# Kernel tuning notes

Hardware: AMD Instinct MI355X
Metric: run time of the kernel (lower is better)

The kernel has to match this reference:

```python
import jax, jax.numpy as jnp
import numpy as np
import math

BS = 8
ROI = 512
D = 1024     # box_feat_dim
G = 16       # group
DH = D // G  # group_feat_dim = 64
GEO = 64     # geo_feat_dim


def setup_inputs() -> dict:
    key = jax.random.key(0)
    ks = jax.random.split(key, 12)
    n = BS * ROI
    box_appearance_feat = jax.random.normal(ks[0], (n, D), dtype=jnp.float32)
    # valid boxes: x2 > x1, y2 > y1, w > 0 (needed for log(w / w^T))
    x1 = jax.random.uniform(ks[1], (n, 1), minval=0.0, maxval=0.5)
    y1 = jax.random.uniform(ks[2], (n, 1), minval=0.0, maxval=0.5)
    w = jax.random.uniform(ks[3], (n, 1), minval=0.05, maxval=0.5)
    h = jax.random.uniform(ks[4], (n, 1), minval=0.05, maxval=0.5)
    boxes = jnp.concatenate([x1, y1, x1 + w, y1 + h], axis=1)
    sc = lambda fan: 1.0 / math.sqrt(fan)
    W_geo = jax.random.normal(ks[5], (GEO, 4), dtype=jnp.float32) * sc(4)
    b_geo = jnp.zeros((GEO,), dtype=jnp.float32)
    W_bgc = jax.random.normal(ks[6], (G, GEO), dtype=jnp.float32) * sc(GEO)  # 1x1 conv GEO->G
    b_bgc = jnp.zeros((G,), dtype=jnp.float32)
    W_q = jax.random.normal(ks[7], (D, D), dtype=jnp.float32) * sc(D)
    b_q = jnp.zeros((D,), dtype=jnp.float32)
    W_k = jax.random.normal(ks[8], (D, D), dtype=jnp.float32) * sc(D)
    b_k = jnp.zeros((D,), dtype=jnp.float32)
    # grouped 1x1 conv G*D -> D with groups=G: per-group linear D -> DH
    W_gc = jax.random.normal(ks[9], (G, DH, D), dtype=jnp.float32) * sc(D)
    b_gc = jnp.zeros((D,), dtype=jnp.float32)
    return {
        "box_appearance_feat": box_appearance_feat, "boxes": boxes,
        "W_geo": W_geo, "b_geo": b_geo, "W_bgc": W_bgc, "b_bgc": b_bgc,
        "W_q": W_q, "b_q": b_q, "W_k": W_k, "b_k": b_k,
        "W_gc": W_gc, "b_gc": b_gc, "bs": BS,
    }


def geometric_encoding(boxes):
    # boxes: [bs, N, 4] -> [bs, N, N, 4]
    x1, y1, x2, y2 = (boxes[..., i] for i in range(4))  # [bs, N]
    w = x2 - x1
    h = y2 - y1
    cx = 0.5 * (x1 + x2)
    cy = 0.5 * (y1 + y2)
    # row-wise division by w_i (torch broadcasts [N,1] over columns)
    dx = (cx[:, :, None] - cx[:, None, :]) / w[:, :, None]
    dx = jnp.log(jnp.maximum(jnp.abs(dx), 1e-3))
    dy = (cy[:, :, None] - cy[:, None, :]) / w[:, :, None]
    dy = jnp.log(jnp.maximum(jnp.abs(dy), 1e-3))
    dw = jnp.log(w[:, :, None] / w[:, None, :])
    dh = jnp.log(h[:, :, None] / h[:, None, :])
    return jnp.stack([dx, dy, dw, dh], axis=-1)


def reference(box_appearance_feat, boxes, W_geo, b_geo, W_bgc, b_bgc,
              W_q, b_q, W_k, b_k, W_gc, b_gc, bs):
    n_total = box_appearance_feat.shape[0]
    roi = n_total // bs
    enc = geometric_encoding(boxes.reshape(bs, roi, 4))            # [b, i, j, 4]
    geo = jnp.tanh(enc @ W_geo.T + b_geo)                          # [b, i, j, GEO]
    # 1x1 conv (GEO -> G) + ReLU (mmcv ConvModule default act), then permute to [b, i, g, j]
    geo_wg = jax.nn.relu(jnp.einsum('bijd,gd->bigj', geo, W_bgc)
                         + b_bgc[None, None, :, None])
    x = box_appearance_feat.reshape(bs, roi, D)
    q = (x @ W_q.T + b_q).reshape(bs, roi, G, DH)
    k = (x @ W_k.T + b_k).reshape(bs, roi, G, DH)
    logits = jnp.einsum('bngd,bmgd->bngm', q, k) / math.sqrt(DH)   # [b, n, g, m]
    weighted = jnp.log(jnp.maximum(geo_wg, 1e-6)) + logits
    sm = jax.nn.softmax(weighted, axis=-1)                         # [b, n, g, m]
    out = jnp.einsum('bngm,bmd->bngd', sm, x)                      # [b, n, g, D]
    # grouped 1x1 conv (G*D -> D, groups=G) + ReLU
    out = jax.nn.relu(jnp.einsum('bngd,god->bngo', out, W_gc)
                      + b_gc.reshape(G, DH))
    return out.reshape(bs * roi, D)
```

## Files before the change

kernel.cpp:

```cpp
#include <hip/hip_runtime.h>
#include <math.h>
#include <stdint.h>


using f16   = _Float16;
using f16x4 = __attribute__((ext_vector_type(4))) f16;
using f16x8 = __attribute__((ext_vector_type(8))) f16;
using f32x4 = __attribute__((ext_vector_type(4))) float;

__device__ __forceinline__ float hw_exp2(float x) { return __builtin_amdgcn_exp2f(x); }
__device__ __forceinline__ float hw_log2(float x) { return __builtin_amdgcn_logf(x); }

__device__ __forceinline__ void cp16(void* lds, const void* g) {
    __builtin_amdgcn_global_load_lds(
        (const __attribute__((address_space(1))) uint32_t*)g,
        (__attribute__((address_space(3))) uint32_t*)lds, 16, 0, 0);
}

__global__ __launch_bounds__(256) void geom_kernel(
    const float* __restrict__ boxes,
    float* __restrict__ gcx, float* __restrict__ gcy,
    float* __restrict__ gw,  float* __restrict__ glw, float* __restrict__ glh)
{
    const int i = blockIdx.x * 256 + threadIdx.x;
    if (i >= 4096) return;
    const float x1 = boxes[i * 4 + 0];
    const float y1 = boxes[i * 4 + 1];
    const float x2 = boxes[i * 4 + 2];
    const float y2 = boxes[i * 4 + 3];
    const float w = x2 - x1, h = y2 - y1;
    gcx[i] = 0.5f * (x1 + x2);
    gcy[i] = 0.5f * (y1 + y2);
    gw[i]  = w;
    glw[i] = logf(w);
    glh[i] = logf(h);
}

__global__ __launch_bounds__(256) void ab_kernel(
    const float* __restrict__ glw, const float* __restrict__ glh,
    const float* __restrict__ W_geo, const float* __restrict__ b_geo,
    float* __restrict__ ABa, float* __restrict__ ABb)
{
    const int i = (blockIdx.x << 2) + (threadIdx.x >> 6);
    const int d = threadIdx.x & 63;
    const float4 wr = *reinterpret_cast<const float4*>(W_geo + (d << 2));
    const float lw = glw[i], lh = glh[i];
    const float bv = fmaf(lw, wr.z, lh * wr.w);
    ABb[i * 64 + d] = bv;
    ABa[i * 64 + d] = bv + b_geo[d] - lw * (wr.x + wr.y);
}

__device__ __forceinline__ void pack_row1(const float* __restrict__ src,
                                          f16* __restrict__ dst, int m, int tid)
{
    const int k = tid << 2;
    const float4 v = *reinterpret_cast<const float4*>(src + (size_t)m * 1024 + k);
    f16x4 a;
    a[0] = (f16)v.x; a[1] = (f16)v.y; a[2] = (f16)v.z; a[3] = (f16)v.w;
    const int sw = (m & 7) << 3;
    *reinterpret_cast<f16x4*>(dst + (size_t)m * 1024 + (k & ~63) + ((k & 63) ^ sw)) = a;
}

__global__ __launch_bounds__(256) void pack4_kernel(
    const float* __restrict__ x,  const float* __restrict__ Wq,
    const float* __restrict__ Wk, const float* __restrict__ Wg,
    f16* __restrict__ xs, f16* __restrict__ wqs,
    f16* __restrict__ wks, f16* __restrict__ wgs)
{
    const int bid = blockIdx.x;
    const float* src; f16* dst; int m;
    if (bid < 4096)      { src = x;  dst = xs;  m = bid; }
    else if (bid < 5120) { src = Wq; dst = wqs; m = bid - 4096; }
    else if (bid < 6144) { src = Wk; dst = wks; m = bid - 5120; }
    else                 { src = Wg; dst = wgs; m = bid - 6144; }
    pack_row1(src, dst, m, threadIdx.x);
}

__global__ __launch_bounds__(256) void packqk_kernel(
    const float* __restrict__ qws, const float* __restrict__ kws,
    f16* __restrict__ qp, f16* __restrict__ kp)
{
    const int bid = blockIdx.x;
    if (bid < 4096) pack_row1(qws, qp, bid, threadIdx.x);
    else            pack_row1(kws, kp, bid - 4096, threadIdx.x);
}

__global__ __launch_bounds__(256) void gemm_qk_f16(
    const f16* __restrict__ xs, const f16* __restrict__ wqs, const f16* __restrict__ wks,
    const float* __restrict__ b_q, const float* __restrict__ b_k,
    float* __restrict__ qout, float* __restrict__ kout)
{
    const bool isK = (blockIdx.z != 0);
    const f16* Bmat   = isK ? wks : wqs;
    const float* bias = isK ? b_k : b_q;
    float* C          = isK ? kout : qout;
    const int m0 = blockIdx.y << 7;
    const int n0 = blockIdx.x << 7;

    __shared__ f16 As[8192];
    __shared__ f16 Bs[8192];

    const int tid  = threadIdx.x;
    const int lane = tid & 63;
    const int w    = tid >> 6;
    const int wr   = (w >> 1) << 6;
    const int wc   = (w & 1) << 6;
    const int srow = lane >> 3;
    const int sseg = (lane & 7) << 4;
    const int l15  = lane & 15;
    const int kgrp = (lane >> 4) << 3;

    f32x4 acc[4][4] = {};

    int aoff[4], boff[4];
    #pragma unroll
    for (int f = 0; f < 4; ++f) {
        const int ra = wr + (f << 4) + l15;
        aoff[f] = (ra << 6) + (kgrp ^ ((ra & 7) << 3));
        const int rb = wc + (f << 4) + l15;
        boff[f] = (rb << 6) + (kgrp ^ ((rb & 7) << 3));
    }

    for (int s = 0; s < 16; ++s) {
        const size_t gb = (size_t)(s << 7) + sseg;
        #pragma unroll
        for (int it = 0; it < 4; ++it) {
            const int ch = (w << 2) + it;
            const int gr = (ch << 3) + srow;
            cp16((char*)As + (ch << 10), (const char*)xs   + (size_t)(m0 + gr) * 2048 + gb);
            cp16((char*)Bs + (ch << 10), (const char*)Bmat + (size_t)(n0 + gr) * 2048 + gb);
        }
        __syncthreads();

        f16x8 a0[4], a1[4], b0[4], b1[4];
        #pragma unroll
        for (int f = 0; f < 4; ++f) {
            a0[f] = *reinterpret_cast<const f16x8*>(As + aoff[f]);
            a1[f] = *reinterpret_cast<const f16x8*>(As + (aoff[f] ^ 32));
            b0[f] = *reinterpret_cast<const f16x8*>(Bs + boff[f]);
            b1[f] = *reinterpret_cast<const f16x8*>(Bs + (boff[f] ^ 32));
        }
        #pragma unroll
        for (int i = 0; i < 4; ++i)
            #pragma unroll
            for (int j = 0; j < 4; ++j) {
                acc[i][j] = __builtin_amdgcn_mfma_f32_16x16x32_f16(a0[i], b0[j], acc[i][j], 0, 0, 0);
                acc[i][j] = __builtin_amdgcn_mfma_f32_16x16x32_f16(a1[i], b1[j], acc[i][j], 0, 0, 0);
            }
        __syncthreads();
    }

    const int rgrp = (lane >> 4) << 2;
    #pragma unroll
    for (int j = 0; j < 4; ++j) {
        const int col = n0 + wc + (j << 4) + l15;
        const float bv = bias[col];
        #pragma unroll
        for (int i = 0; i < 4; ++i) {
            const int row = m0 + wr + (i << 4) + rgrp;
            #pragma unroll
            for (int r = 0; r < 4; ++r)
                C[(size_t)(row + r) * 1024 + col] = acc[i][j][r] + bv;
        }
    }
}

__global__ __launch_bounds__(256) void gemm_yt_f16(
    const f16* __restrict__ xs, const f16* __restrict__ wgs,
    f16* __restrict__ Yt)
{
    const int z = blockIdx.z;
    const int b = z >> 4, g = z & 15;
    const int m0 = blockIdx.y << 7;
    const f16* A    = xs  + (size_t)(b << 9) * 1024;
    const f16* Bmat = wgs + (size_t)(g << 6) * 1024;

    __shared__ f16 As[8192];
    __shared__ f16 Bs[4096];

    const int tid  = threadIdx.x;
    const int lane = tid & 63;
    const int w    = tid >> 6;
    const int wr   = (w >> 1) << 6;
    const int wc   = (w & 1) << 5;
    const int srow = lane >> 3;
    const int sseg = (lane & 7) << 4;
    const int l15  = lane & 15;
    const int kgrp = (lane >> 4) << 3;

    f32x4 acc[4][2] = {};

    int aoff[4], boff[2];
    #pragma unroll
    for (int f = 0; f < 4; ++f) {
        const int ra = wr + (f << 4) + l15;
        aoff[f] = (ra << 6) + (kgrp ^ ((ra & 7) << 3));
    }
    #pragma unroll
    for (int f = 0; f < 2; ++f) {
        const int rb = wc + (f << 4) + l15;
        boff[f] = (rb << 6) + (kgrp ^ ((rb & 7) << 3));
    }

    for (int s = 0; s < 16; ++s) {
        const size_t gb = (size_t)(s << 7) + sseg;
        #pragma unroll
        for (int it = 0; it < 4; ++it) {
            const int ch = (w << 2) + it;
            cp16((char*)As + (ch << 10),
                 (const char*)A + (size_t)(m0 + (ch << 3) + srow) * 2048 + gb);
        }
        #pragma unroll
        for (int it = 0; it < 2; ++it) {
            const int ch = (w << 1) + it;
            cp16((char*)Bs + (ch << 10),
                 (const char*)Bmat + (size_t)((ch << 3) + srow) * 2048 + gb);
        }
        __syncthreads();

        f16x8 a0[4], a1[4], b0[2], b1[2];
        #pragma unroll
        for (int f = 0; f < 4; ++f) {
            a0[f] = *reinterpret_cast<const f16x8*>(As + aoff[f]);
            a1[f] = *reinterpret_cast<const f16x8*>(As + (aoff[f] ^ 32));
        }
        #pragma unroll
        for (int f = 0; f < 2; ++f) {
            b0[f] = *reinterpret_cast<const f16x8*>(Bs + boff[f]);
            b1[f] = *reinterpret_cast<const f16x8*>(Bs + (boff[f] ^ 32));
        }
        #pragma unroll
        for (int i = 0; i < 4; ++i)
            #pragma unroll
            for (int j = 0; j < 2; ++j) {
                acc[i][j] = __builtin_amdgcn_mfma_f32_16x16x32_f16(b0[j], a0[i], acc[i][j], 0, 0, 0);
                acc[i][j] = __builtin_amdgcn_mfma_f32_16x16x32_f16(b1[j], a1[i], acc[i][j], 0, 0, 0);
            }
        __syncthreads();
    }

    const int rgrp = (lane >> 4) << 2;
    #pragma unroll
    for (int jj = 0; jj < 2; ++jj) {
        const int obase = wc + (jj << 4) + rgrp;
        #pragma unroll
        for (int i = 0; i < 4; ++i) {
            const int jcol = m0 + wr + (i << 4) + l15;
            const int jhi = (jcol >> 6) << 6, jlo = jcol & 63;
            #pragma unroll
            for (int r = 0; r < 4; ++r) {
                const int o = obase + r;
                Yt[((size_t)z << 15) + (o << 9) + jhi + (jlo ^ ((o & 7) << 3))]
                    = (f16)acc[i][jj][r];
            }
        }
    }
}

__global__ __launch_bounds__(256, 4) void geo_mfma(
    const float* __restrict__ gcx, const float* __restrict__ gcy,
    const float* __restrict__ gw,
    const float* __restrict__ ABa, const float* __restrict__ ABb,
    const float* __restrict__ W_geo, const float* __restrict__ W_bgc,
    const float* __restrict__ b_bgc,
    f16* __restrict__ S)
{
    __shared__ float2 sJ[512];

    const int tid  = threadIdx.x;
    const int lane = tid & 63;
    const int h    = lane >> 4;
    const int p    = lane & 15;
    const int w    = tid >> 6;
    const int bb   = blockIdx.y;
    const int irow = (blockIdx.x << 2) + w;
    const int ig   = (bb << 9) + irow;
    const float LN2 = 0.69314718056f;

    float2 wA[8], wB[8];
    #pragma unroll
    for (int e = 0; e < 8; ++e) {
        const float4 t0 = *reinterpret_cast<const float4*>(W_geo + (((h << 3) + e) << 2));
        wA[e] = make_float2(t0.x * LN2, t0.y * LN2);
        const float4 t1 = *reinterpret_cast<const float4*>(W_geo + ((32 + (h << 3) + e) << 2));
        wB[e] = make_float2(t1.x * LN2, t1.y * LN2);
    }
    float aiA[8], aiB[8];
    {
        const float4 a0 = *reinterpret_cast<const float4*>(ABa + ig * 64 + (h << 3));
        const float4 a1 = *reinterpret_cast<const float4*>(ABa + ig * 64 + (h << 3) + 4);
        aiA[0] = a0.x; aiA[1] = a0.y; aiA[2] = a0.z; aiA[3] = a0.w;
        aiA[4] = a1.x; aiA[5] = a1.y; aiA[6] = a1.z; aiA[7] = a1.w;
        const float4 b0 = *reinterpret_cast<const float4*>(ABa + ig * 64 + 32 + (h << 3));
        const float4 b1 = *reinterpret_cast<const float4*>(ABa + ig * 64 + 32 + (h << 3) + 4);
        aiB[0] = b0.x; aiB[1] = b0.y; aiB[2] = b0.z; aiB[3] = b0.w;
        aiB[4] = b1.x; aiB[5] = b1.y; aiB[6] = b1.z; aiB[7] = b1.w;
    }
    f16x8 wbh0, wbl0, wbh1, wbl1;
    #pragma unroll
    for (int e = 0; e < 8; ++e) {
        const float v0 = W_bgc[(p << 6) + (h << 3) + e];
        const f16 x0 = (f16)v0; wbh0[e] = x0; wbl0[e] = (f16)(v0 - (float)x0);
        const float v1 = W_bgc[(p << 6) + 32 + (h << 3) + e];
        const f16 x1 = (f16)v1; wbh1[e] = x1; wbl1[e] = (f16)(v1 - (float)x1);
    }
    const float bbias = b_bgc[p];
    const float cxi = gcx[ig], cyi = gcy[ig];
    const float ti  = 1e-3f * gw[ig];

    for (int l = tid; l < 512; l += 256) {
        const int jg = (bb << 9) + l;
        sJ[l] = make_float2(gcx[jg], gcy[jg]);
    }
    __syncthreads();

    const float* bjrow = ABb + ((size_t)(bb << 9) << 6) + (p << 6) + (h << 3);
    float4 cA0 = *reinterpret_cast<const float4*>(bjrow);
    float4 cA1 = *reinterpret_cast<const float4*>(bjrow + 4);
    float4 cB0 = *reinterpret_cast<const float4*>(bjrow + 32);
    float4 cB1 = *reinterpret_cast<const float4*>(bjrow + 36);

    f16* sp = S + (((size_t)((bb << 4) + p)) << 18) + ((size_t)irow << 9) + (h << 2);

    for (int jc = 0; jc < 32; ++jc) {
        float4 nA0, nA1, nB0, nB1;
        if (jc < 31) {
            const float* nx = bjrow + ((jc + 1) << 10);
            nA0 = *reinterpret_cast<const float4*>(nx);
            nA1 = *reinterpret_cast<const float4*>(nx + 4);
            nB0 = *reinterpret_cast<const float4*>(nx + 32);
            nB1 = *reinterpret_cast<const float4*>(nx + 36);
        }
        const float2 je = sJ[(jc << 4) + p];
        const float e0 = hw_log2(fmaxf(fabsf(cxi - je.x), ti));
        const float e1 = hw_log2(fmaxf(fabsf(cyi - je.y), ti));

        const float bjA[8] = {cA0.x, cA0.y, cA0.z, cA0.w, cA1.x, cA1.y, cA1.z, cA1.w};
        const float bjB[8] = {cB0.x, cB0.y, cB0.z, cB0.w, cB1.x, cB1.y, cB1.z, cB1.w};

        f16x8 hhA, hlA, hhB, hlB;
        #pragma unroll
        for (int e = 0; e < 8; ++e) {
            float t = fmaf(e0, wA[e].x, fmaf(e1, wA[e].y, aiA[e] - bjA[e]));
            t = fmaf(-2.0f, __builtin_amdgcn_rcpf(hw_exp2(t * 2.885390082f) + 1.0f), 1.0f);
            const f16 a = (f16)t; hhA[e] = a; hlA[e] = (f16)(t - (float)a);
            float u = fmaf(e0, wB[e].x, fmaf(e1, wB[e].y, aiB[e] - bjB[e]));
            u = fmaf(-2.0f, __builtin_amdgcn_rcpf(hw_exp2(u * 2.885390082f) + 1.0f), 1.0f);
            const f16 c = (f16)u; hhB[e] = c; hlB[e] = (f16)(u - (float)c);
        }
        f32x4 acc = {0.f, 0.f, 0.f, 0.f};
        acc = __builtin_amdgcn_mfma_f32_16x16x32_f16(hhA, wbh0, acc, 0, 0, 0);
        acc = __builtin_amdgcn_mfma_f32_16x16x32_f16(hlA, wbh0, acc, 0, 0, 0);
        acc = __builtin_amdgcn_mfma_f32_16x16x32_f16(hhA, wbl0, acc, 0, 0, 0);
        acc = __builtin_amdgcn_mfma_f32_16x16x32_f16(hhB, wbh1, acc, 0, 0, 0);
        acc = __builtin_amdgcn_mfma_f32_16x16x32_f16(hlB, wbh1, acc, 0, 0, 0);
        acc = __builtin_amdgcn_mfma_f32_16x16x32_f16(hhB, wbl1, acc, 0, 0, 0);

        f16x4 o4;
        #pragma unroll
        for (int r = 0; r < 4; ++r)
            o4[r] = (f16)fmaxf(acc[r] + bbias, 1e-6f);
        *reinterpret_cast<f16x4*>(sp + (jc << 4)) = o4;

        cA0 = nA0; cA1 = nA1; cB0 = nB0; cB1 = nB1;
    }
}

__global__ __launch_bounds__(256) void attn_fused(
    const f16* __restrict__ qp, const f16* __restrict__ kp,
    const f16* __restrict__ Sb, const f16* __restrict__ Yt,
    const float* __restrict__ b_gc, float* __restrict__ out)
{
    __shared__ float Ss[16][514];
    __shared__ f16   P[16 * 512];

    const int tid  = threadIdx.x;
    const int lane = tid & 63;
    const int w    = tid >> 6;
    const int h    = lane >> 4;
    const int p_   = lane & 15;
    const int kgrp = h << 3;
    const int i0   = blockIdx.x << 4;
    const int z    = blockIdx.y;
    const int b    = z >> 4, g = z & 15;

    const char* qbytes = (const char*)qp + ((size_t)((b << 9) + i0)) * 2048 + (g << 7);
    const char* kbytes = (const char*)kp + ((size_t)(b << 9)) * 2048 + (g << 7);

    f16x8 aq[2];
    {
        const char* qrow = qbytes + (size_t)p_ * 2048;
        #pragma unroll
        for (int s = 0; s < 2; ++s) {
            const int bo = ((s << 5) + kgrp) ^ ((p_ & 7) << 3);
            aq[s] = *reinterpret_cast<const f16x8*>(qrow + bo * 2);
        }
    }

    #pragma unroll
    for (int f = 0; f < 8; ++f) {
        const int j = (w << 7) + (f << 4) + p_;
        const char* krow = kbytes + (size_t)j * 2048;
        f32x4 a = {0.f, 0.f, 0.f, 0.f};
        #pragma unroll
        for (int s = 0; s < 2; ++s) {
            const int bo = ((s << 5) + kgrp) ^ ((j & 7) << 3);
            const f16x8 bk = *reinterpret_cast<const f16x8*>(krow + bo * 2);
            a = __builtin_amdgcn_mfma_f32_16x16x32_f16(aq[s], bk, a, 0, 0, 0);
        }
        #pragma unroll
        for (int r = 0; r < 4; ++r)
            Ss[(h << 2) + r][(w << 7) + (f << 4) + p_] = 0.125f * a[r];
    }
    __syncthreads();

    #pragma unroll
    for (int rr = 0; rr < 4; ++rr) {
        const int row = (w << 2) + rr;
        const f16* wbp = Sb + ((size_t)z << 18) + ((size_t)(i0 + row) << 9);
        float l[8];
        float m = -3.0e38f;
        #pragma unroll
        for (int t = 0; t < 8; ++t) { l[t] = Ss[row][(t << 6) + lane]; m = fmaxf(m, l[t]); }
        #pragma unroll
        for (int off = 32; off > 0; off >>= 1) m = fmaxf(m, __shfl_xor(m, off));
        float wb[8];
        #pragma unroll
        for (int t = 0; t < 8; ++t) wb[t] = (float)wbp[(t << 6) + lane];
        float ssum = 0.f;
        #pragma unroll
        for (int t = 0; t < 8; ++t) { l[t] = wb[t] * __expf(l[t] - m); ssum += l[t]; }
        #pragma unroll
        for (int off = 32; off > 0; off >>= 1) ssum += __shfl_xor(ssum, off);
        const float inv = 1.0f / ssum;
        const int sw = (row & 7) << 3;
        f16* prow = P + (row << 9);
        #pragma unroll
        for (int t = 0; t < 8; ++t)
            prow[(t << 6) + (lane ^ sw)] = (f16)(l[t] * inv);
    }
    __syncthreads();

    const int o = (w << 4) + p_;
    const f16* ytz = Yt + ((size_t)z << 15) + ((size_t)o << 9);
    const f16* pr  = P + (p_ << 9);
    f32x4 av = {0.f, 0.f, 0.f, 0.f};
    #pragma unroll
    for (int t = 0; t < 8; ++t) {
        #pragma unroll
        for (int s = 0; s < 2; ++s) {
            const int ko = (s << 5) + kgrp;
            const f16x8 bf = *reinterpret_cast<const f16x8*>(ytz + (t << 6) + (ko ^ ((o  & 7) << 3)));
            const f16x8 af = *reinterpret_cast<const f16x8*>(pr  + (t << 6) + (ko ^ ((p_ & 7) << 3)));
            av = __builtin_amdgcn_mfma_f32_16x16x32_f16(af, bf, av, 0, 0, 0);
        }
    }
    const float bg = b_gc[(g << 6) + o];
    float* orow = out + ((size_t)((b << 9) + i0)) * 1024 + (g << 6) + o;
    #pragma unroll
    for (int r = 0; r < 4; ++r)
        orow[(size_t)((h << 2) + r) * 1024] = fmaxf(av[r] + bg, 0.f);
}

extern "C" void kernel_launch(void* const* d_in, const int* in_sizes, int n_in,
                              void* d_out, int out_size, void* d_ws, size_t ws_size,
                              hipStream_t stream)
{
    (void)in_sizes; (void)n_in; (void)out_size; (void)ws_size;
    const float* x     = (const float*)d_in[0];
    const float* boxes = (const float*)d_in[1];
    const float* W_geo = (const float*)d_in[2];
    const float* b_geo = (const float*)d_in[3];
    const float* W_bgc = (const float*)d_in[4];
    const float* b_bgc = (const float*)d_in[5];
    const float* W_q   = (const float*)d_in[6];
    const float* b_q   = (const float*)d_in[7];
    const float* W_k   = (const float*)d_in[8];
    const float* b_k   = (const float*)d_in[9];
    const float* W_gc  = (const float*)d_in[10];
    const float* b_gc  = (const float*)d_in[11];
    float* out = (float*)d_out;

    float* fws = (float*)d_ws;
    float* gcx = fws;
    float* gcy = gcx + 4096;
    float* gw  = gcy + 4096;
    float* glw = gw  + 4096;
    float* glh = glw + 4096;
    float* ABa = glh + 4096;
    float* ABb = ABa + 4096 * 64;
    f16* qp  = (f16*)(ABb + 4096 * 64);
    f16* kp  = qp + (size_t)4096 * 1024;
    f16* ytp = kp + (size_t)4096 * 1024;
    f16* Sws = ytp + (size_t)128 * 64 * 512;

    f16* xs  = Sws;
    f16* wqs = xs  + (size_t)4096 * 1024;
    f16* wks = wqs + (size_t)1024 * 1024;
    f16* wgs = wks + (size_t)1024 * 1024;
    float* qws = (float*)(wgs + (size_t)1024 * 1024);
    float* kws = qws + (size_t)4096 * 1024;

    geom_kernel<<<16, 256, 0, stream>>>(boxes, gcx, gcy, gw, glw, glh);
    ab_kernel<<<1024, 256, 0, stream>>>(glw, glh, W_geo, b_geo, ABa, ABb);
    pack4_kernel<<<7168, 256, 0, stream>>>(x, W_q, W_k, W_gc, xs, wqs, wks, wgs);
    gemm_qk_f16<<<dim3(8, 32, 2), 256, 0, stream>>>(xs, wqs, wks, b_q, b_k, qws, kws);
    packqk_kernel<<<8192, 256, 0, stream>>>(qws, kws, qp, kp);
    gemm_yt_f16<<<dim3(1, 4, 128), 256, 0, stream>>>(xs, wgs, ytp);
    geo_mfma<<<dim3(128, 8), 256, 0, stream>>>(gcx, gcy, gw, ABa, ABb,
                                               W_geo, W_bgc, b_bgc, Sws);
    attn_fused<<<dim3(32, 128), 256, 0, stream>>>(qp, kp, Sws, ytp, b_gc, out);
}
```

Baseline: 270.3 us.

## Fuse Q/K fp16 swizzled packing into GEMM epilogue and transpose geo MFMA output

The Q/K GEMM now writes its biased results straight to fp16 in the swizzled layout the attention kernel expects. This removes the fp32 intermediate buffers and the separate packqk launch, saving a full fp32 write and read of two 4096x1024 matrices. The geo_mfma kernel swaps the MFMA operand order so each lane's accumulator holds four groups for one column, and it writes scalar fp16 stores across group planes instead of one f16x4 vector store. The epilogue stores are scalar 2-byte writes with XOR-swizzled columns, which may coalesce less well.

```diff
diff --git a/kernel.cpp b/kernel.cpp
--- a/kernel.cpp
+++ b/kernel.cpp
@@ -76,24 +76,15 @@
     pack_row1(src, dst, m, threadIdx.x);
 }
 
-__global__ __launch_bounds__(256) void packqk_kernel(
-    const float* __restrict__ qws, const float* __restrict__ kws,
-    f16* __restrict__ qp, f16* __restrict__ kp)
-{
-    const int bid = blockIdx.x;
-    if (bid < 4096) pack_row1(qws, qp, bid, threadIdx.x);
-    else            pack_row1(kws, kp, bid - 4096, threadIdx.x);
-}
-
 __global__ __launch_bounds__(256) void gemm_qk_f16(
     const f16* __restrict__ xs, const f16* __restrict__ wqs, const f16* __restrict__ wks,
     const float* __restrict__ b_q, const float* __restrict__ b_k,
-    float* __restrict__ qout, float* __restrict__ kout)
+    f16* __restrict__ qp, f16* __restrict__ kp)
 {
     const bool isK = (blockIdx.z != 0);
     const f16* Bmat   = isK ? wks : wqs;
     const float* bias = isK ? b_k : b_q;
-    float* C          = isK ? kout : qout;
+    f16* Cp           = isK ? kp : qp;
     const int m0 = blockIdx.y << 7;
     const int n0 = blockIdx.x << 7;
 
@@ -155,12 +146,16 @@
     for (int j = 0; j < 4; ++j) {
         const int col = n0 + wc + (j << 4) + l15;
         const float bv = bias[col];
+        const int chi = col & ~63, clo = col & 63;
         #pragma unroll
         for (int i = 0; i < 4; ++i) {
             const int row = m0 + wr + (i << 4) + rgrp;
             #pragma unroll
-            for (int r = 0; r < 4; ++r)
-                C[(size_t)(row + r) * 1024 + col] = acc[i][j][r] + bv;
+            for (int r = 0; r < 4; ++r) {
+                const int rr = row + r;
+                const int sw = (rr & 7) << 3;
+                Cp[(size_t)rr * 1024 + chi + (clo ^ sw)] = (f16)(acc[i][j][r] + bv);
+            }
         }
     }
 }
@@ -304,7 +299,10 @@
         const float v1 = W_bgc[(p << 6) + 32 + (h << 3) + e];
         const f16 x1 = (f16)v1; wbh1[e] = x1; wbl1[e] = (f16)(v1 - (float)x1);
     }
-    const float bbias = b_bgc[p];
+    float bb4[4];
+    #pragma unroll
+    for (int r = 0; r < 4; ++r) bb4[r] = b_bgc[(h << 2) + r];
+
     const float cxi = gcx[ig], cyi = gcy[ig];
     const float ti  = 1e-3f * gw[ig];
 
@@ -320,7 +318,7 @@
     float4 cB0 = *reinterpret_cast<const float4*>(bjrow + 32);
     float4 cB1 = *reinterpret_cast<const float4*>(bjrow + 36);
 
-    f16* sp = S + (((size_t)((bb << 4) + p)) << 18) + ((size_t)irow << 9) + (h << 2);
+    f16* sp = S + (((size_t)((bb << 4) + (h << 2))) << 18) + ((size_t)irow << 9) + p;
 
     for (int jc = 0; jc < 32; ++jc) {
         float4 nA0, nA1, nB0, nB1;
@@ -349,18 +347,16 @@
             const f16 c = (f16)u; hhB[e] = c; hlB[e] = (f16)(u - (float)c);
         }
         f32x4 acc = {0.f, 0.f, 0.f, 0.f};
-        acc = __builtin_amdgcn_mfma_f32_16x16x32_f16(hhA, wbh0, acc, 0, 0, 0);
-        acc = __builtin_amdgcn_mfma_f32_16x16x32_f16(hlA, wbh0, acc, 0, 0, 0);
-        acc = __builtin_amdgcn_mfma_f32_16x16x32_f16(hhA, wbl0, acc, 0, 0, 0);
-        acc = __builtin_amdgcn_mfma_f32_16x16x32_f16(hhB, wbh1, acc, 0, 0, 0);
-        acc = __builtin_amdgcn_mfma_f32_16x16x32_f16(hlB, wbh1, acc, 0, 0, 0);
-        acc = __builtin_amdgcn_mfma_f32_16x16x32_f16(hhB, wbl1, acc, 0, 0, 0);
-
-        f16x4 o4;
+        acc = __builtin_amdgcn_mfma_f32_16x16x32_f16(wbh0, hhA, acc, 0, 0, 0);
+        acc = __builtin_amdgcn_mfma_f32_16x16x32_f16(wbh0, hlA, acc, 0, 0, 0);
+        acc = __builtin_amdgcn_mfma_f32_16x16x32_f16(wbl0, hhA, acc, 0, 0, 0);
+        acc = __builtin_amdgcn_mfma_f32_16x16x32_f16(wbh1, hhB, acc, 0, 0, 0);
+        acc = __builtin_amdgcn_mfma_f32_16x16x32_f16(wbh1, hlB, acc, 0, 0, 0);
+        acc = __builtin_amdgcn_mfma_f32_16x16x32_f16(wbl1, hhB, acc, 0, 0, 0);
+
         #pragma unroll
         for (int r = 0; r < 4; ++r)
-            o4[r] = (f16)fmaxf(acc[r] + bbias, 1e-6f);
-        *reinterpret_cast<f16x4*>(sp + (jc << 4)) = o4;
+            sp[((size_t)r << 18) + (jc << 4)] = (f16)fmaxf(acc[r] + bb4[r], 1e-6f);
 
         cA0 = nA0; cA1 = nA1; cB0 = nB0; cB1 = nB1;
     }
@@ -498,14 +494,11 @@
     f16* wqs = xs  + (size_t)4096 * 1024;
     f16* wks = wqs + (size_t)1024 * 1024;
     f16* wgs = wks + (size_t)1024 * 1024;
-    float* qws = (float*)(wgs + (size_t)1024 * 1024);
-    float* kws = qws + (size_t)4096 * 1024;
 
     geom_kernel<<<16, 256, 0, stream>>>(boxes, gcx, gcy, gw, glw, glh);
     ab_kernel<<<1024, 256, 0, stream>>>(glw, glh, W_geo, b_geo, ABa, ABb);
     pack4_kernel<<<7168, 256, 0, stream>>>(x, W_q, W_k, W_gc, xs, wqs, wks, wgs);
-    gemm_qk_f16<<<dim3(8, 32, 2), 256, 0, stream>>>(xs, wqs, wks, b_q, b_k, qws, kws);
-    packqk_kernel<<<8192, 256, 0, stream>>>(qws, kws, qp, kp);
+    gemm_qk_f16<<<dim3(8, 32, 2), 256, 0, stream>>>(xs, wqs, wks, b_q, b_k, qp, kp);
     gemm_yt_f16<<<dim3(1, 4, 128), 256, 0, stream>>>(xs, wgs, ytp);
     geo_mfma<<<dim3(128, 8), 256, 0, stream>>>(gcx, gcy, gw, ABa, ABb,
                                                W_geo, W_bgc, b_bgc, Sws);
```

After: 254.2 us. 6.0% less time.
